# Optimization experiments

Measured on AMD Instinct MI355X. Metric: run time of the kernel, lower is better.

## Reference

```python
import jax, jax.numpy as jnp
import numpy as np

B, T, E, H, K, V = 256, 200, 100, 128, 13, 50000


def run_lstm(x, W, U, b, reverse=False):
    """Keras LSTM with activation=relu, recurrent_activation=sigmoid.
    x: [B,T,E]; W: [E,4H]; U: [H,4H]; b: [4H]. Gate order: i, f, g, o.
    Returns hidden states [B,T,H] (time-aligned for both directions)."""
    Bn = x.shape[0]
    Hn = U.shape[0]
    xw = jnp.einsum('bte,eg->btg', x, W) + b  # precompute input projections [B,T,4H]

    def step(carry, xw_t):
        h, c = carry
        z = xw_t + h @ U
        i, f, g, o = jnp.split(z, 4, axis=-1)
        i = jax.nn.sigmoid(i)
        f = jax.nn.sigmoid(f)
        g = jax.nn.relu(g)          # activation=relu (non-cuDNN path in TF)
        c = f * c + i * g
        h = o * jax.nn.relu(c)      # output activation also relu
        return (h, c), h

    init = (jnp.zeros((Bn, Hn), x.dtype), jnp.zeros((Bn, Hn), x.dtype))
    _, hs = jax.lax.scan(step, init, jnp.swapaxes(xw, 0, 1), reverse=reverse)
    return jnp.swapaxes(hs, 0, 1)


def crf_log_likelihood(logits, labels, lens, trans):
    """tfa.text.crf_log_likelihood: score(labels) - logZ, masked by seq lens."""
    Bn, Tn, Kn = logits.shape
    t_idx = jnp.arange(Tn)
    mask = t_idx[None, :] < lens[:, None]  # [B,T]
    # unary score
    unary = jnp.take_along_axis(logits, labels[..., None], axis=-1)[..., 0]
    u_score = jnp.sum(jnp.where(mask, unary, 0.0), axis=-1)
    # transition score
    pair = trans[labels[:, :-1], labels[:, 1:]]  # [B,T-1]
    pmask = t_idx[None, 1:] < lens[:, None]
    b_score = jnp.sum(jnp.where(pmask, pair, 0.0), axis=-1)
    # forward algorithm (log-space DP over time, masked updates)
    def step(alpha, inp):
        logit_t, valid = inp  # [B,K], [B]
        new = jax.nn.logsumexp(alpha[:, :, None] + trans[None], axis=1) + logit_t
        alpha = jnp.where(valid[:, None], new, alpha)
        return alpha, None

    alpha0 = logits[:, 0, :]
    xs = (jnp.swapaxes(logits[:, 1:, :], 0, 1), jnp.swapaxes(mask[:, 1:], 0, 1))
    alpha, _ = jax.lax.scan(step, alpha0, xs)
    logZ = jax.nn.logsumexp(alpha, axis=-1)
    return u_score + b_score - logZ


def setup_inputs() -> dict:
    key = jax.random.key(0)
    ks = jax.random.split(key, 12)
    s = lambda k, shape, sc: jax.random.normal(k, shape, jnp.float32) * sc
    return {
        'text': jax.random.randint(ks[0], (B, T), 0, V).astype(jnp.int32),
        'labels': jax.random.randint(ks[1], (B, T), 0, K).astype(jnp.int32),
        'emb': s(ks[2], (V, E), 0.1),
        'Wf': s(ks[3], (E, 4 * H), 0.05),
        'Uf': s(ks[4], (H, 4 * H), 0.05),
        'bf': jnp.zeros((4 * H,), jnp.float32),
        'Wb': s(ks[5], (E, 4 * H), 0.05),
        'Ub': s(ks[6], (H, 4 * H), 0.05),
        'bb': jnp.zeros((4 * H,), jnp.float32),
        'Wd': s(ks[7], (2 * H, K), 0.05),
        'bd': jnp.zeros((K,), jnp.float32),
        'trans': jax.random.uniform(ks[8], (K, K), jnp.float32),
    }


def reference(text, labels, emb, Wf, Uf, bf, Wb, Ub, bb, Wd, bd, trans):
    lens = jnp.sum((text != 0).astype(jnp.int32), axis=-1)  # [B]
    x = emb[text]                      # embedding lookup [B,T,E]
    # dropout is identity in eval mode
    h_fwd = run_lstm(x, Wf, Uf, bf, reverse=False)
    h_bwd = run_lstm(x, Wb, Ub, bb, reverse=True)
    h = jnp.concatenate([h_fwd, h_bwd], axis=-1)  # [B,T,2H]
    logits = jax.nn.softmax(h @ Wd + bd, axis=-1)  # Dense(softmax), per source
    log_likelihood = crf_log_likelihood(logits, labels, lens, trans)
    return logits, lens, log_likelihood
```

## Files before the change

kernel.cpp:

```cpp
#include <hip/hip_runtime.h>
#include <hip/hip_bf16.h>

#define Bn 256
#define Tn 200
#define En 100
#define Hn 128
#define Kn 13
#define G4 512
#define BT 51200

typedef __attribute__((ext_vector_type(8))) __bf16 bf8_t;
typedef __attribute__((ext_vector_type(4))) float f4_t;

__device__ __forceinline__ unsigned short f2bf(float f) {
  unsigned int u = __float_as_uint(f);
  u = (u + 0x7FFFu + ((u >> 16) & 1u)) >> 16;
  return (unsigned short)u;
}
__device__ __forceinline__ float bf2f(unsigned short s) {
  return __uint_as_float(((unsigned int)s) << 16);
}
__device__ __forceinline__ float sigm(float x) { return 1.f / (1.f + __expf(-x)); }

__device__ __forceinline__ void bar_lgkm() {
  asm volatile("s_waitcnt lgkmcnt(0)" ::: "memory");
  __builtin_amdgcn_s_barrier();
  __builtin_amdgcn_sched_barrier(0);
}

__device__ __forceinline__ int gperm(int n) {
  return ((n >> 4) & 3) * 128 + ((n >> 6) << 4) + (n & 15);
}

__global__ __launch_bounds__(256) void k_prep(const int* __restrict__ text,
                                              const float* __restrict__ Wf,
                                              const float* __restrict__ Wb,
                                              const float* __restrict__ Uf,
                                              const float* __restrict__ Ub,
                                              unsigned short* __restrict__ wt,
                                              unsigned short* __restrict__ ut,
                                              int* __restrict__ lens_i,
                                              float* __restrict__ out_lens) {
  int bx = blockIdx.x;
  if (bx < 1024) {
    int idx = bx * 256 + threadIdx.x;
    int half = idx >> 17;
    int rem = idx & 131071;
    int dir = rem >> 16;
    int nk = rem & 65535;
    int n = nk >> 7, k = nk & 127;
    int mc = gperm(n);
    if (half == 0) {
      const float* W = dir ? Wb : Wf;
      wt[rem] = f2bf((k < En) ? W[k * G4 + mc] : 0.f);
    } else {
      const float* U = dir ? Ub : Uf;
      ut[rem] = f2bf(U[k * G4 + mc]);
    }
  } else {
    int wi = threadIdx.x >> 6, lane = threadIdx.x & 63;
    int b = (bx - 1024) * 4 + wi;
    int cnt = 0;
    for (int t = lane; t < Tn; t += 64) cnt += (text[b * Tn + t] != 0);
    for (int off = 32; off; off >>= 1) cnt += __shfl_down(cnt, off);
    if (lane == 0) { lens_i[b] = cnt; out_lens[b] = (float)cnt; }
  }
}

#define FR16(M) M(0,0) M(0,1) M(0,2) M(0,3) M(1,0) M(1,1) M(1,2) M(1,3) \
                M(2,0) M(2,1) M(2,2) M(2,3) M(3,0) M(3,1) M(3,2) M(3,3)

__global__ __attribute__((amdgpu_flat_work_group_size(512, 512),
                          amdgpu_waves_per_eu(1, 2)))
void k_scan(const int* __restrict__ text,
            const float* __restrict__ emb,
            const unsigned short* __restrict__ wt,
            const unsigned short* __restrict__ ut,
            const float* __restrict__ biasf,
            const float* __restrict__ biasb,
            unsigned short* __restrict__ hf,
            unsigned short* __restrict__ hb) {
  int blk = blockIdx.x;
  int dir = blk >> 6;
  int bg = blk & 63;
  int b0 = bg * 4;
  int tid = threadIdx.x;
  int w = tid >> 6, l = tid & 63;
  int lr = l & 15, lg = l >> 4;
  int jj = w * 16 + lr;
  const unsigned short* ut_d = ut + (size_t)dir * (G4 * 128);
  const unsigned short* wt_d = wt + (size_t)dir * (G4 * 128);
  const float* bias = dir ? biasb : biasf;
  unsigned short* hout = dir ? hb : hf;
  int t0 = dir ? (Tn - 1) : 0;
  int dt = dir ? -1 : 1;

#define LOADUB(nt, kk) \
  bf8_t ub_##nt##_##kk = *(const bf8_t*)(ut_d + (size_t)(w * 64 + (nt) * 16 + lr) * 128 + (kk) * 32 + lg * 8); \
  asm volatile("" : "+a"(ub_##nt##_##kk));
  FR16(LOADUB)
#undef LOADUB
#define LOADWB(nt, kk) \
  bf8_t wb_##nt##_##kk = *(const bf8_t*)(wt_d + (size_t)(w * 64 + (nt) * 16 + lr) * 128 + (kk) * 32 + lg * 8); \
  asm volatile("" : "+a"(wb_##nt##_##kk));
  FR16(LOADWB)
#undef LOADWB

  __shared__ __align__(16) char lds_all[16384 + Tn * 4 * 4];
  char* lbase = lds_all;
  int* tl = (int*)(lds_all + 16384);
  for (int i = tid; i < 4096; i += 512) ((unsigned int*)lds_all)[i] = 0;
  #pragma unroll
  for (int r = 0; r < 4; r++)
    if (tid < Tn) tl[r * Tn + tid] = text[(size_t)(b0 + r) * Tn + tid];

  float bn0 = bias[gperm(w * 64 +  0 + lr)];
  float bn1 = bias[gperm(w * 64 + 16 + lr)];
  float bn2 = bias[gperm(w * 64 + 32 + lr)];
  float bn3 = bias[gperm(w * 64 + 48 + lr)];
  f4_t bv0 = {bn0, bn0, bn0, bn0};
  f4_t bv1 = {bn1, bn1, bn1, bn1};
  f4_t bv2 = {bn2, bn2, bn2, bn2};
  f4_t bv3 = {bn3, bn3, bn3, bn3};

  int xrow = tid >> 7;
  int xcol = tid & 127;
  bool xon = (xcol < En);
  float v0 = 0.f, v1 = 0.f, vA = 0.f, vB = 0.f;
  {
    const int* trow = text + (size_t)(b0 + xrow) * Tn;
    int k0 = trow[t0], k1 = trow[t0 + dt], k2 = trow[t0 + 2 * dt], k3 = trow[t0 + 3 * dt];
    if (xon) {
      v0 = emb[(size_t)k0 * En + xcol];
      v1 = emb[(size_t)k1 * En + xcol];
      vA = emb[(size_t)k2 * En + xcol];
      vB = emb[(size_t)k3 * En + xcol];
    }
  }

  int rb0 = (lr * 256 +   0 + lg * 16) ^ ((lr & 7) << 4);
  int rb1 = (lr * 256 +  64 + lg * 16) ^ ((lr & 7) << 4);
  int rb2 = (lr * 256 + 128 + lg * 16) ^ ((lr & 7) << 4);
  int rb3 = (lr * 256 + 192 + lg * 16) ^ ((lr & 7) << 4);
  int xb0 = 12288 + rb0, xb1 = 12288 + rb1, xb2 = 12288 + rb2, xb3 = 12288 + rb3;
  int wbh = (((lg * 4) * 256 + jj * 2) ^ (((lg * 4) & 7) << 4)) + 4096;
  int wbx = 8192 + (((xrow * 4) * 256 + xcol * 2) ^ (((xrow * 4) & 7) << 4));

  unsigned short* hp = hout + ((size_t)t0 * Bn + b0 + lg) * 128 + jj;
  const long long hstep = (long long)dt * Bn * 128;

  *(unsigned short*)(lbase + wbx) = f2bf(v0);
  *(unsigned short*)(lbase + (wbx ^ 4096)) = f2bf(v1);
  bar_lgkm();

  f4_t pA0 = bv0, pA1 = bv1, pA2 = bv2, pA3 = bv3;
  f4_t pB0, pB1, pB2, pB3;
  {
    bf8_t ax0 = *(const bf8_t*)(lbase + 8192 + rb0);
    bf8_t ax1 = *(const bf8_t*)(lbase + 8192 + rb1);
    bf8_t ax2 = *(const bf8_t*)(lbase + 8192 + rb2);
    bf8_t ax3 = *(const bf8_t*)(lbase + 8192 + rb3);
#define MFP(nt, kk) pA##nt = __builtin_amdgcn_mfma_f32_16x16x32_bf16(ax##kk, wb_##nt##_##kk, pA##nt, 0, 0, 0);
    MFP(0,0) MFP(1,0) MFP(2,0) MFP(3,0)
    MFP(0,1) MFP(1,1) MFP(2,1) MFP(3,1)
    MFP(0,2) MFP(1,2) MFP(2,2) MFP(3,2)
    MFP(0,3) MFP(1,3) MFP(2,3) MFP(3,3)
#undef MFP
  }
  float c0 = 0.f;
  int t = t0;

#define STEPF(P, Q) { \
    bf8_t af0 = *(const bf8_t*)(lbase + rb0); \
    bf8_t af1 = *(const bf8_t*)(lbase + rb1); \
    bf8_t af2 = *(const bf8_t*)(lbase + rb2); \
    bf8_t af3 = *(const bf8_t*)(lbase + rb3); \
     \
    *(unsigned short*)(lbase + wbx) = f2bf(vA); \
    vA = vB; \
    { int tc = t + 3 * dt; tc = tc < 0 ? 0 : (tc > Tn - 1 ? Tn - 1 : tc); \
      int tokN = tl[xrow * Tn + tc]; \
      vB = xon ? emb[(size_t)tokN * En + xcol] : 0.f; } \
     \
    P##0 = __builtin_amdgcn_mfma_f32_16x16x32_bf16(af0, ub_0_0, P##0, 0, 0, 0); \
    P##1 = __builtin_amdgcn_mfma_f32_16x16x32_bf16(af0, ub_1_0, P##1, 0, 0, 0); \
    P##2 = __builtin_amdgcn_mfma_f32_16x16x32_bf16(af0, ub_2_0, P##2, 0, 0, 0); \
    P##3 = __builtin_amdgcn_mfma_f32_16x16x32_bf16(af0, ub_3_0, P##3, 0, 0, 0); \
    P##0 = __builtin_amdgcn_mfma_f32_16x16x32_bf16(af1, ub_0_1, P##0, 0, 0, 0); \
    P##1 = __builtin_amdgcn_mfma_f32_16x16x32_bf16(af1, ub_1_1, P##1, 0, 0, 0); \
    P##2 = __builtin_amdgcn_mfma_f32_16x16x32_bf16(af1, ub_2_1, P##2, 0, 0, 0); \
    P##3 = __builtin_amdgcn_mfma_f32_16x16x32_bf16(af1, ub_3_1, P##3, 0, 0, 0); \
    P##0 = __builtin_amdgcn_mfma_f32_16x16x32_bf16(af2, ub_0_2, P##0, 0, 0, 0); \
    P##1 = __builtin_amdgcn_mfma_f32_16x16x32_bf16(af2, ub_1_2, P##1, 0, 0, 0); \
    P##2 = __builtin_amdgcn_mfma_f32_16x16x32_bf16(af2, ub_2_2, P##2, 0, 0, 0); \
    P##3 = __builtin_amdgcn_mfma_f32_16x16x32_bf16(af2, ub_3_2, P##3, 0, 0, 0); \
    P##0 = __builtin_amdgcn_mfma_f32_16x16x32_bf16(af3, ub_0_3, P##0, 0, 0, 0); \
    P##1 = __builtin_amdgcn_mfma_f32_16x16x32_bf16(af3, ub_1_3, P##1, 0, 0, 0); \
    P##2 = __builtin_amdgcn_mfma_f32_16x16x32_bf16(af3, ub_2_3, P##2, 0, 0, 0); \
    P##3 = __builtin_amdgcn_mfma_f32_16x16x32_bf16(af3, ub_3_3, P##3, 0, 0, 0); \
     \
    { bf8_t ax0 = *(const bf8_t*)(lbase + xb0); \
      bf8_t ax1 = *(const bf8_t*)(lbase + xb1); \
      bf8_t ax2 = *(const bf8_t*)(lbase + xb2); \
      bf8_t ax3 = *(const bf8_t*)(lbase + xb3); \
      Q##0 = bv0; Q##1 = bv1; Q##2 = bv2; Q##3 = bv3; \
      Q##0 = __builtin_amdgcn_mfma_f32_16x16x32_bf16(ax0, wb_0_0, Q##0, 0, 0, 0); \
      Q##1 = __builtin_amdgcn_mfma_f32_16x16x32_bf16(ax0, wb_1_0, Q##1, 0, 0, 0); \
      Q##2 = __builtin_amdgcn_mfma_f32_16x16x32_bf16(ax0, wb_2_0, Q##2, 0, 0, 0); \
      Q##3 = __builtin_amdgcn_mfma_f32_16x16x32_bf16(ax0, wb_3_0, Q##3, 0, 0, 0); \
      Q##0 = __builtin_amdgcn_mfma_f32_16x16x32_bf16(ax1, wb_0_1, Q##0, 0, 0, 0); \
      Q##1 = __builtin_amdgcn_mfma_f32_16x16x32_bf16(ax1, wb_1_1, Q##1, 0, 0, 0); \
      Q##2 = __builtin_amdgcn_mfma_f32_16x16x32_bf16(ax1, wb_2_1, Q##2, 0, 0, 0); \
      Q##3 = __builtin_amdgcn_mfma_f32_16x16x32_bf16(ax1, wb_3_1, Q##3, 0, 0, 0); \
      Q##0 = __builtin_amdgcn_mfma_f32_16x16x32_bf16(ax2, wb_0_2, Q##0, 0, 0, 0); \
      Q##1 = __builtin_amdgcn_mfma_f32_16x16x32_bf16(ax2, wb_1_2, Q##1, 0, 0, 0); \
      Q##2 = __builtin_amdgcn_mfma_f32_16x16x32_bf16(ax2, wb_2_2, Q##2, 0, 0, 0); \
      Q##3 = __builtin_amdgcn_mfma_f32_16x16x32_bf16(ax2, wb_3_2, Q##3, 0, 0, 0); \
      Q##0 = __builtin_amdgcn_mfma_f32_16x16x32_bf16(ax3, wb_0_3, Q##0, 0, 0, 0); \
      Q##1 = __builtin_amdgcn_mfma_f32_16x16x32_bf16(ax3, wb_1_3, Q##1, 0, 0, 0); \
      Q##2 = __builtin_amdgcn_mfma_f32_16x16x32_bf16(ax3, wb_2_3, Q##2, 0, 0, 0); \
      Q##3 = __builtin_amdgcn_mfma_f32_16x16x32_bf16(ax3, wb_3_3, Q##3, 0, 0, 0); } \
     \
    float ig = sigm(P##0[0]); \
    float fg = sigm(P##1[0]); \
    float gg = fmaxf(P##2[0], 0.f); \
    c0 = fmaf(fg, c0, ig * gg); \
    unsigned short hs2 = f2bf(sigm(P##3[0]) * fmaxf(c0, 0.f)); \
    *(unsigned short*)(lbase + wbh) = hs2; \
    bar_lgkm(); \
    hp[0] = hs2; \
    rb0 ^= 4096; rb1 ^= 4096; rb2 ^= 4096; rb3 ^= 4096; \
    xb0 ^= 4096; xb1 ^= 4096; xb2 ^= 4096; xb3 ^= 4096; \
    wbh ^= 4096; wbx ^= 4096; \
    hp += hstep; \
    t += dt; }

  for (int tt = 0; tt < Tn; tt += 2) {
    STEPF(pA, pB)
    STEPF(pB, pA)
  }
#undef STEPF
}

__global__ __launch_bounds__(128) void k_logits(const unsigned short* __restrict__ hf,
                                                const unsigned short* __restrict__ hb,
                                                const float* __restrict__ Wd,
                                                const float* __restrict__ bd,
                                                float* __restrict__ out) {
  __shared__ unsigned short hs[128 * 256];
  int tid = threadIdx.x;
  size_t row0 = (size_t)blockIdx.x * 128;
  #pragma unroll
  for (int it = 0; it < 16; it++) {
    int idx = it * 128 + tid;
    int r = idx >> 4, c = idx & 15;
    bf8_t vf = *(const bf8_t*)(hf + (row0 + r) * 128 + c * 8);
    bf8_t vb = *(const bf8_t*)(hb + (row0 + r) * 128 + c * 8);
    int byte = (r * 512 + c * 16) ^ ((r & 7) << 4);
    *(bf8_t*)((char*)hs + byte) = vf;
    int byte2 = (r * 512 + 256 + c * 16) ^ ((r & 7) << 4);
    *(bf8_t*)((char*)hs + byte2) = vb;
  }
  __syncthreads();
  float acc[Kn];
  #pragma unroll
  for (int jj = 0; jj < Kn; jj++) acc[jj] = bd[jj];
  int r = tid;
  #pragma unroll 4
  for (int c = 0; c < 32; c++) {
    int byte = (r * 512 + c * 16) ^ ((r & 7) << 4);
    bf8_t v = *(const bf8_t*)((const char*)hs + byte);
    #pragma unroll
    for (int e = 0; e < 8; e++) {
      float h = (float)v[e];
      int k = c * 8 + e;
      #pragma unroll
      for (int jj = 0; jj < Kn; jj++)
        acc[jj] = fmaf(h, Wd[k * Kn + jj], acc[jj]);
    }
  }
  float m = acc[0];
  #pragma unroll
  for (int jj = 1; jj < Kn; jj++) m = fmaxf(m, acc[jj]);
  float s = 0.f;
  #pragma unroll
  for (int jj = 0; jj < Kn; jj++) { acc[jj] = __expf(acc[jj] - m); s += acc[jj]; }
  float inv = 1.f / s;
  int rg = (int)row0 + tid;
  int b = rg & 255, t = rg >> 8;
  float* op = out + ((size_t)b * Tn + t) * Kn;
  #pragma unroll
  for (int jj = 0; jj < Kn; jj++) op[jj] = acc[jj] * inv;
}

__global__ __launch_bounds__(64) void k_crf(const float* __restrict__ logits,
                                            const int* __restrict__ labels,
                                            const int* __restrict__ lens_i,
                                            const float* __restrict__ trans,
                                            float* __restrict__ out_ll) {
  int b = blockIdx.x, lane = threadIdx.x;
  int len = lens_i[b];
  const float* lg = logits + (size_t)b * Tn * Kn;
  const int* lab = labels + (size_t)b * Tn;
  float sc = 0.f;
  for (int t = lane; t < Tn; t += 64) {
    if (t < len) {
      sc += lg[t * Kn + lab[t]];
      if (t >= 1) sc += trans[lab[t - 1] * Kn + lab[t]];
    }
  }
  for (int off = 32; off; off >>= 1) sc += __shfl_down(sc, off);
  bool act = lane < Kn;
  int jl = act ? lane : 0;
  float etr[Kn];
  #pragma unroll
  for (int i = 0; i < Kn; i++) etr[i] = __expf(trans[i * Kn + jl]);
  float a = act ? lg[jl] : -INFINITY;
  float lgv = (len > 1) ? lg[Kn + jl] : 0.f;
  for (int t = 1; t < len; t++) {
    float lgn = (t + 1 < len) ? lg[(t + 1) * Kn + jl] : 0.f;
    float m = a;
    for (int off = 8; off; off >>= 1) m = fmaxf(m, __shfl_xor(m, off, 16));
    float ea = __expf(a - m);
    float s = 0.f;
    #pragma unroll
    for (int i = 0; i < Kn; i++) s = fmaf(__shfl(ea, i), etr[i], s);
    float anew = m + __logf(s) + lgv;
    if (act) a = anew;
    lgv = lgn;
  }
  float m2 = a;
  for (int off = 8; off; off >>= 1) m2 = fmaxf(m2, __shfl_xor(m2, off, 16));
  float ea2 = act ? __expf(a - m2) : 0.f;
  float ssum = ea2;
  for (int off = 8; off; off >>= 1) ssum += __shfl_xor(ssum, off, 16);
  float logZ = m2 + __logf(ssum);
  if (lane == 0) out_ll[b] = sc - logZ;
}

extern "C" void kernel_launch(void* const* d_in, const int* in_sizes, int n_in,
                              void* d_out, int out_size, void* d_ws, size_t ws_size,
                              hipStream_t stream) {
  const int* text = (const int*)d_in[0];
  const int* labels = (const int*)d_in[1];
  const float* emb = (const float*)d_in[2];
  const float* Wf = (const float*)d_in[3];
  const float* Uf = (const float*)d_in[4];
  const float* bf_ = (const float*)d_in[5];
  const float* Wb = (const float*)d_in[6];
  const float* Ub = (const float*)d_in[7];
  const float* bb_ = (const float*)d_in[8];
  const float* Wd = (const float*)d_in[9];
  const float* bd = (const float*)d_in[10];
  const float* trans = (const float*)d_in[11];
  (void)in_sizes; (void)n_in; (void)out_size; (void)ws_size;

  float* out = (float*)d_out;
  float* out_logits = out;
  float* out_lens = out + (size_t)BT * Kn;
  float* out_ll = out_lens + Bn;

  char* ws = (char*)d_ws;
  size_t o = 0;
  int* lens_i = (int*)(ws + o);                o += 1024;
  unsigned short* wt = (unsigned short*)(ws + o);  o += (size_t)2 * G4 * 128 * 2;
  unsigned short* ut = (unsigned short*)(ws + o);  o += (size_t)2 * G4 * 128 * 2;
  unsigned short* hfb = (unsigned short*)(ws + o); o += (size_t)BT * Hn * 2;
  unsigned short* hbb = (unsigned short*)(ws + o); o += (size_t)BT * Hn * 2;

  hipLaunchKernelGGL(k_prep, dim3(1088), dim3(256), 0, stream,
                     text, Wf, Wb, Uf, Ub, wt, ut, lens_i, out_lens);
  hipLaunchKernelGGL(k_scan, dim3(128), dim3(512), 0, stream,
                     text, emb, wt, ut, bf_, bb_, hfb, hbb);
  hipLaunchKernelGGL(k_logits, dim3(400), dim3(128), 0, stream, hfb, hbb, Wd, bd, out_logits);
  hipLaunchKernelGGL(k_crf, dim3(Bn), dim3(64), 0, stream, out_logits, labels, lens_i, trans, out_ll);
}
```

Before: 285.2 us.

## Halve scan block to 4 waves, each computing 8 gate tiles

The LSTM scan kernel now runs with 256 threads per block instead of 512. Each wave covers 32 hidden units, using 8 MFMA N-tiles with doubled U and W register fragments, and each thread handles two embedding rows. The aim is to cut the per-step barrier cost across fewer waves and give each wave more independent MFMA chains to hide latency. In exchange, each wave carries twice the serial MFMA and activation work per step and much higher register pressure (64 bf8 weight fragments).

Measured after the change: 326.8 us. +14.6%, slower.

```diff
diff --git a/kernel.cpp b/kernel.cpp
--- a/kernel.cpp
+++ b/kernel.cpp
@@ -31,6 +31,8 @@
 __device__ __forceinline__ int gperm(int n) {
   return ((n >> 4) & 3) * 128 + ((n >> 6) << 4) + (n & 15);
 }
+
+#define MFMA(a, b, c) __builtin_amdgcn_mfma_f32_16x16x32_bf16(a, b, c, 0, 0, 0)
 
 __global__ __launch_bounds__(256) void k_prep(const int* __restrict__ text,
                                               const float* __restrict__ Wf,
@@ -67,11 +69,43 @@
   }
 }
 
-#define FR16(M) M(0,0) M(0,1) M(0,2) M(0,3) M(1,0) M(1,1) M(1,2) M(1,3) \
-                M(2,0) M(2,1) M(2,2) M(2,3) M(3,0) M(3,1) M(3,2) M(3,3)
-
-__global__ __attribute__((amdgpu_flat_work_group_size(512, 512),
-                          amdgpu_waves_per_eu(1, 2)))
+#define NT8K4(M) M(0,0) M(0,1) M(0,2) M(0,3) M(1,0) M(1,1) M(1,2) M(1,3) \
+                 M(2,0) M(2,1) M(2,2) M(2,3) M(3,0) M(3,1) M(3,2) M(3,3) \
+                 M(4,0) M(4,1) M(4,2) M(4,3) M(5,0) M(5,1) M(5,2) M(5,3) \
+                 M(6,0) M(6,1) M(6,2) M(6,3) M(7,0) M(7,1) M(7,2) M(7,3)
+
+#define MFUK(P, kk) \
+    P##0 = MFMA(af##kk, ub_0_##kk, P##0); \
+    P##1 = MFMA(af##kk, ub_1_##kk, P##1); \
+    P##2 = MFMA(af##kk, ub_2_##kk, P##2); \
+    P##3 = MFMA(af##kk, ub_3_##kk, P##3); \
+    P##4 = MFMA(af##kk, ub_4_##kk, P##4); \
+    P##5 = MFMA(af##kk, ub_5_##kk, P##5); \
+    P##6 = MFMA(af##kk, ub_6_##kk, P##6); \
+    P##7 = MFMA(af##kk, ub_7_##kk, P##7);
+
+#define MFW0(Q) \
+    Q##0 = MFMA(ax0, wb_0_0, bv0); \
+    Q##1 = MFMA(ax0, wb_1_0, bv1); \
+    Q##2 = MFMA(ax0, wb_2_0, bv2); \
+    Q##3 = MFMA(ax0, wb_3_0, bv3); \
+    Q##4 = MFMA(ax0, wb_4_0, bv4); \
+    Q##5 = MFMA(ax0, wb_5_0, bv5); \
+    Q##6 = MFMA(ax0, wb_6_0, bv6); \
+    Q##7 = MFMA(ax0, wb_7_0, bv7);
+
+#define MFWK(Q, kk) \
+    Q##0 = MFMA(ax##kk, wb_0_##kk, Q##0); \
+    Q##1 = MFMA(ax##kk, wb_1_##kk, Q##1); \
+    Q##2 = MFMA(ax##kk, wb_2_##kk, Q##2); \
+    Q##3 = MFMA(ax##kk, wb_3_##kk, Q##3); \
+    Q##4 = MFMA(ax##kk, wb_4_##kk, Q##4); \
+    Q##5 = MFMA(ax##kk, wb_5_##kk, Q##5); \
+    Q##6 = MFMA(ax##kk, wb_6_##kk, Q##6); \
+    Q##7 = MFMA(ax##kk, wb_7_##kk, Q##7);
+
+__global__ __attribute__((amdgpu_flat_work_group_size(256, 256),
+                          amdgpu_waves_per_eu(1, 1)))
 void k_scan(const int* __restrict__ text,
             const float* __restrict__ emb,
             const unsigned short* __restrict__ wt,
@@ -87,7 +121,7 @@
   int tid = threadIdx.x;
   int w = tid >> 6, l = tid & 63;
   int lr = l & 15, lg = l >> 4;
-  int jj = w * 16 + lr;
+  int j0 = w * 32 + lr;
   const unsigned short* ut_d = ut + (size_t)dir * (G4 * 128);
   const unsigned short* wt_d = wt + (size_t)dir * (G4 * 128);
   const float* bias = dir ? biasb : biasf;
@@ -96,45 +130,49 @@
   int dt = dir ? -1 : 1;
 
 #define LOADUB(nt, kk) \
-  bf8_t ub_##nt##_##kk = *(const bf8_t*)(ut_d + (size_t)(w * 64 + (nt) * 16 + lr) * 128 + (kk) * 32 + lg * 8); \
+  bf8_t ub_##nt##_##kk = *(const bf8_t*)(ut_d + (size_t)(w * 128 + (nt) * 16 + lr) * 128 + (kk) * 32 + lg * 8); \
   asm volatile("" : "+a"(ub_##nt##_##kk));
-  FR16(LOADUB)
+  NT8K4(LOADUB)
 #undef LOADUB
 #define LOADWB(nt, kk) \
-  bf8_t wb_##nt##_##kk = *(const bf8_t*)(wt_d + (size_t)(w * 64 + (nt) * 16 + lr) * 128 + (kk) * 32 + lg * 8); \
+  bf8_t wb_##nt##_##kk = *(const bf8_t*)(wt_d + (size_t)(w * 128 + (nt) * 16 + lr) * 128 + (kk) * 32 + lg * 8); \
   asm volatile("" : "+a"(wb_##nt##_##kk));
-  FR16(LOADWB)
+  NT8K4(LOADWB)
 #undef LOADWB
 
   __shared__ __align__(16) char lds_all[16384 + Tn * 4 * 4];
   char* lbase = lds_all;
   int* tl = (int*)(lds_all + 16384);
-  for (int i = tid; i < 4096; i += 512) ((unsigned int*)lds_all)[i] = 0;
+  for (int i = tid; i < 4096; i += 256) ((unsigned int*)lds_all)[i] = 0;
   #pragma unroll
   for (int r = 0; r < 4; r++)
     if (tid < Tn) tl[r * Tn + tid] = text[(size_t)(b0 + r) * Tn + tid];
 
-  float bn0 = bias[gperm(w * 64 +  0 + lr)];
-  float bn1 = bias[gperm(w * 64 + 16 + lr)];
-  float bn2 = bias[gperm(w * 64 + 32 + lr)];
-  float bn3 = bias[gperm(w * 64 + 48 + lr)];
-  f4_t bv0 = {bn0, bn0, bn0, bn0};
-  f4_t bv1 = {bn1, bn1, bn1, bn1};
-  f4_t bv2 = {bn2, bn2, bn2, bn2};
-  f4_t bv3 = {bn3, bn3, bn3, bn3};
-
-  int xrow = tid >> 7;
-  int xcol = tid & 127;
-  bool xon = (xcol < En);
-  float v0 = 0.f, v1 = 0.f, vA = 0.f, vB = 0.f;
+  f4_t bv0, bv1, bv2, bv3, bv4, bv5, bv6, bv7;
+#define LBIAS(nt) { float b_ = bias[gperm(w * 128 + (nt) * 16 + lr)]; \
+  bv##nt[0] = b_; bv##nt[1] = b_; bv##nt[2] = b_; bv##nt[3] = b_; }
+  LBIAS(0) LBIAS(1) LBIAS(2) LBIAS(3) LBIAS(4) LBIAS(5) LBIAS(6) LBIAS(7)
+#undef LBIAS
+
+  int xr0 = tid >> 7;
+  int xc = tid & 127;
+  bool xon = (xc < En);
+  float v00 = 0.f, v01 = 0.f;
+  float v10 = 0.f, v11 = 0.f;
+  float vA0 = 0.f, vA1 = 0.f;
+  float vB0 = 0.f, vB1 = 0.f;
   {
-    const int* trow = text + (size_t)(b0 + xrow) * Tn;
-    int k0 = trow[t0], k1 = trow[t0 + dt], k2 = trow[t0 + 2 * dt], k3 = trow[t0 + 3 * dt];
+    const int* tr0 = text + (size_t)(b0 + xr0) * Tn;
+    const int* tr1 = text + (size_t)(b0 + xr0 + 2) * Tn;
     if (xon) {
-      v0 = emb[(size_t)k0 * En + xcol];
-      v1 = emb[(size_t)k1 * En + xcol];
-      vA = emb[(size_t)k2 * En + xcol];
-      vB = emb[(size_t)k3 * En + xcol];
+      v00 = emb[(size_t)tr0[t0] * En + xc];
+      v01 = emb[(size_t)tr1[t0] * En + xc];
+      v10 = emb[(size_t)tr0[t0 + dt] * En + xc];
+      v11 = emb[(size_t)tr1[t0 + dt] * En + xc];
+      vA0 = emb[(size_t)tr0[t0 + 2 * dt] * En + xc];
+      vA1 = emb[(size_t)tr1[t0 + 2 * dt] * En + xc];
+      vB0 = emb[(size_t)tr0[t0 + 3 * dt] * En + xc];
+      vB1 = emb[(size_t)tr1[t0 + 3 * dt] * En + xc];
     }
   }
 
@@ -143,31 +181,34 @@
   int rb2 = (lr * 256 + 128 + lg * 16) ^ ((lr & 7) << 4);
   int rb3 = (lr * 256 + 192 + lg * 16) ^ ((lr & 7) << 4);
   int xb0 = 12288 + rb0, xb1 = 12288 + rb1, xb2 = 12288 + rb2, xb3 = 12288 + rb3;
-  int wbh = (((lg * 4) * 256 + jj * 2) ^ (((lg * 4) & 7) << 4)) + 4096;
-  int wbx = 8192 + (((xrow * 4) * 256 + xcol * 2) ^ (((xrow * 4) & 7) << 4));
-
-  unsigned short* hp = hout + ((size_t)t0 * Bn + b0 + lg) * 128 + jj;
+  int hrow = lg * 4;
+  int hsw = ((hrow & 7) << 4);
+  int wbh0 = ((hrow * 256 + j0 * 2) ^ hsw) + 4096;
+  int wbh1 = ((hrow * 256 + (j0 + 16) * 2) ^ hsw) + 4096;
+  int xrow0b = (xr0 * 4) * 256;
+  int xrow1b = ((xr0 + 2) * 4) * 256;
+  int wbx0 = 8192 + ((xrow0b + xc * 2) ^ (((xr0 * 4) & 7) << 4));
+  int wbx1 = 8192 + ((xrow1b + xc * 2) ^ ((((xr0 + 2) * 4) & 7) << 4));
+
+  unsigned short* hp = hout + ((size_t)t0 * Bn + b0 + lg) * 128 + j0;
   const long long hstep = (long long)dt * Bn * 128;
 
-  *(unsigned short*)(lbase + wbx) = f2bf(v0);
-  *(unsigned short*)(lbase + (wbx ^ 4096)) = f2bf(v1);
+  *(unsigned short*)(lbase + wbx0) = f2bf(v00);
+  *(unsigned short*)(lbase + wbx1) = f2bf(v01);
+  *(unsigned short*)(lbase + (wbx0 ^ 4096)) = f2bf(v10);
+  *(unsigned short*)(lbase + (wbx1 ^ 4096)) = f2bf(v11);
   bar_lgkm();
 
-  f4_t pA0 = bv0, pA1 = bv1, pA2 = bv2, pA3 = bv3;
-  f4_t pB0, pB1, pB2, pB3;
+  f4_t pA0, pA1, pA2, pA3, pA4, pA5, pA6, pA7;
+  f4_t pB0, pB1, pB2, pB3, pB4, pB5, pB6, pB7;
   {
     bf8_t ax0 = *(const bf8_t*)(lbase + 8192 + rb0);
     bf8_t ax1 = *(const bf8_t*)(lbase + 8192 + rb1);
     bf8_t ax2 = *(const bf8_t*)(lbase + 8192 + rb2);
     bf8_t ax3 = *(const bf8_t*)(lbase + 8192 + rb3);
-#define MFP(nt, kk) pA##nt = __builtin_amdgcn_mfma_f32_16x16x32_bf16(ax##kk, wb_##nt##_##kk, pA##nt, 0, 0, 0);
-    MFP(0,0) MFP(1,0) MFP(2,0) MFP(3,0)
-    MFP(0,1) MFP(1,1) MFP(2,1) MFP(3,1)
-    MFP(0,2) MFP(1,2) MFP(2,2) MFP(3,2)
-    MFP(0,3) MFP(1,3) MFP(2,3) MFP(3,3)
-#undef MFP
-  }
-  float c0 = 0.f;
+    MFW0(pA) MFWK(pA, 1) MFWK(pA, 2) MFWK(pA, 3)
+  }
+  float c0 = 0.f, c1 = 0.f;
   int t = t0;
 
 #define STEPF(P, Q) { \
@@ -175,63 +216,41 @@
     bf8_t af1 = *(const bf8_t*)(lbase + rb1); \
     bf8_t af2 = *(const bf8_t*)(lbase + rb2); \
     bf8_t af3 = *(const bf8_t*)(lbase + rb3); \
+    bf8_t ax0 = *(const bf8_t*)(lbase + xb0); \
+    bf8_t ax1 = *(const bf8_t*)(lbase + xb1); \
+    bf8_t ax2 = *(const bf8_t*)(lbase + xb2); \
+    bf8_t ax3 = *(const bf8_t*)(lbase + xb3); \
      \
-    *(unsigned short*)(lbase + wbx) = f2bf(vA); \
-    vA = vB; \
+    *(unsigned short*)(lbase + wbx0) = f2bf(vA0); \
+    *(unsigned short*)(lbase + wbx1) = f2bf(vA1); \
+    vA0 = vB0; vA1 = vB1; \
     { int tc = t + 3 * dt; tc = tc < 0 ? 0 : (tc > Tn - 1 ? Tn - 1 : tc); \
-      int tokN = tl[xrow * Tn + tc]; \
-      vB = xon ? emb[(size_t)tokN * En + xcol] : 0.f; } \
+      int tk0 = tl[xr0 * Tn + tc]; \
+      int tk1 = tl[(xr0 + 2) * Tn + tc]; \
+      vB0 = xon ? emb[(size_t)tk0 * En + xc] : 0.f; \
+      vB1 = xon ? emb[(size_t)tk1 * En + xc] : 0.f; } \
      \
-    P##0 = __builtin_amdgcn_mfma_f32_16x16x32_bf16(af0, ub_0_0, P##0, 0, 0, 0); \
-    P##1 = __builtin_amdgcn_mfma_f32_16x16x32_bf16(af0, ub_1_0, P##1, 0, 0, 0); \
-    P##2 = __builtin_amdgcn_mfma_f32_16x16x32_bf16(af0, ub_2_0, P##2, 0, 0, 0); \
-    P##3 = __builtin_amdgcn_mfma_f32_16x16x32_bf16(af0, ub_3_0, P##3, 0, 0, 0); \
-    P##0 = __builtin_amdgcn_mfma_f32_16x16x32_bf16(af1, ub_0_1, P##0, 0, 0, 0); \
-    P##1 = __builtin_amdgcn_mfma_f32_16x16x32_bf16(af1, ub_1_1, P##1, 0, 0, 0); \
-    P##2 = __builtin_amdgcn_mfma_f32_16x16x32_bf16(af1, ub_2_1, P##2, 0, 0, 0); \
-    P##3 = __builtin_amdgcn_mfma_f32_16x16x32_bf16(af1, ub_3_1, P##3, 0, 0, 0); \
-    P##0 = __builtin_amdgcn_mfma_f32_16x16x32_bf16(af2, ub_0_2, P##0, 0, 0, 0); \
-    P##1 = __builtin_amdgcn_mfma_f32_16x16x32_bf16(af2, ub_1_2, P##1, 0, 0, 0); \
-    P##2 = __builtin_amdgcn_mfma_f32_16x16x32_bf16(af2, ub_2_2, P##2, 0, 0, 0); \
-    P##3 = __builtin_amdgcn_mfma_f32_16x16x32_bf16(af2, ub_3_2, P##3, 0, 0, 0); \
-    P##0 = __builtin_amdgcn_mfma_f32_16x16x32_bf16(af3, ub_0_3, P##0, 0, 0, 0); \
-    P##1 = __builtin_amdgcn_mfma_f32_16x16x32_bf16(af3, ub_1_3, P##1, 0, 0, 0); \
-    P##2 = __builtin_amdgcn_mfma_f32_16x16x32_bf16(af3, ub_2_3, P##2, 0, 0, 0); \
-    P##3 = __builtin_amdgcn_mfma_f32_16x16x32_bf16(af3, ub_3_3, P##3, 0, 0, 0); \
+    MFUK(P, 0) MFUK(P, 1) MFUK(P, 2) MFUK(P, 3) \
      \
-    { bf8_t ax0 = *(const bf8_t*)(lbase + xb0); \
-      bf8_t ax1 = *(const bf8_t*)(lbase + xb1); \
-      bf8_t ax2 = *(const bf8_t*)(lbase + xb2); \
-      bf8_t ax3 = *(const bf8_t*)(lbase + xb3); \
-      Q##0 = bv0; Q##1 = bv1; Q##2 = bv2; Q##3 = bv3; \
-      Q##0 = __builtin_amdgcn_mfma_f32_16x16x32_bf16(ax0, wb_0_0, Q##0, 0, 0, 0); \
-      Q##1 = __builtin_amdgcn_mfma_f32_16x16x32_bf16(ax0, wb_1_0, Q##1, 0, 0, 0); \
-      Q##2 = __builtin_amdgcn_mfma_f32_16x16x32_bf16(ax0, wb_2_0, Q##2, 0, 0, 0); \
-      Q##3 = __builtin_amdgcn_mfma_f32_16x16x32_bf16(ax0, wb_3_0, Q##3, 0, 0, 0); \
-      Q##0 = __builtin_amdgcn_mfma_f32_16x16x32_bf16(ax1, wb_0_1, Q##0, 0, 0, 0); \
-      Q##1 = __builtin_amdgcn_mfma_f32_16x16x32_bf16(ax1, wb_1_1, Q##1, 0, 0, 0); \
-      Q##2 = __builtin_amdgcn_mfma_f32_16x16x32_bf16(ax1, wb_2_1, Q##2, 0, 0, 0); \
-      Q##3 = __builtin_amdgcn_mfma_f32_16x16x32_bf16(ax1, wb_3_1, Q##3, 0, 0, 0); \
-      Q##0 = __builtin_amdgcn_mfma_f32_16x16x32_bf16(ax2, wb_0_2, Q##0, 0, 0, 0); \
-      Q##1 = __builtin_amdgcn_mfma_f32_16x16x32_bf16(ax2, wb_1_2, Q##1, 0, 0, 0); \
-      Q##2 = __builtin_amdgcn_mfma_f32_16x16x32_bf16(ax2, wb_2_2, Q##2, 0, 0, 0); \
-      Q##3 = __builtin_amdgcn_mfma_f32_16x16x32_bf16(ax2, wb_3_2, Q##3, 0, 0, 0); \
-      Q##0 = __builtin_amdgcn_mfma_f32_16x16x32_bf16(ax3, wb_0_3, Q##0, 0, 0, 0); \
-      Q##1 = __builtin_amdgcn_mfma_f32_16x16x32_bf16(ax3, wb_1_3, Q##1, 0, 0, 0); \
-      Q##2 = __builtin_amdgcn_mfma_f32_16x16x32_bf16(ax3, wb_2_3, Q##2, 0, 0, 0); \
-      Q##3 = __builtin_amdgcn_mfma_f32_16x16x32_bf16(ax3, wb_3_3, Q##3, 0, 0, 0); } \
+    MFW0(Q) MFWK(Q, 1) MFWK(Q, 2) MFWK(Q, 3) \
      \
-    float ig = sigm(P##0[0]); \
-    float fg = sigm(P##1[0]); \
-    float gg = fmaxf(P##2[0], 0.f); \
-    c0 = fmaf(fg, c0, ig * gg); \
-    unsigned short hs2 = f2bf(sigm(P##3[0]) * fmaxf(c0, 0.f)); \
-    *(unsigned short*)(lbase + wbh) = hs2; \
+    float ig0 = sigm(P##0[0]); \
+    float fg0 = sigm(P##1[0]); \
+    float gg0 = fmaxf(P##2[0], 0.f); \
+    c0 = fmaf(fg0, c0, ig0 * gg0); \
+    unsigned short h0s = f2bf(sigm(P##3[0]) * fmaxf(c0, 0.f)); \
+    float ig1 = sigm(P##4[0]); \
+    float fg1 = sigm(P##5[0]); \
+    float gg1 = fmaxf(P##6[0], 0.f); \
+    c1 = fmaf(fg1, c1, ig1 * gg1); \
+    unsigned short h1s = f2bf(sigm(P##7[0]) * fmaxf(c1, 0.f)); \
+    *(unsigned short*)(lbase + wbh0) = h0s; \
+    *(unsigned short*)(lbase + wbh1) = h1s; \
     bar_lgkm(); \
-    hp[0] = hs2; \
+    hp[0] = h0s; hp[16] = h1s; \
     rb0 ^= 4096; rb1 ^= 4096; rb2 ^= 4096; rb3 ^= 4096; \
     xb0 ^= 4096; xb1 ^= 4096; xb2 ^= 4096; xb3 ^= 4096; \
-    wbh ^= 4096; wbx ^= 4096; \
+    wbh0 ^= 4096; wbh1 ^= 4096; wbx0 ^= 4096; wbx1 ^= 4096; \
     hp += hstep; \
     t += dt; }
 
@@ -370,7 +389,7 @@
 
   hipLaunchKernelGGL(k_prep, dim3(1088), dim3(256), 0, stream,
                      text, Wf, Wb, Uf, Ub, wt, ut, lens_i, out_lens);
-  hipLaunchKernelGGL(k_scan, dim3(128), dim3(512), 0, stream,
+  hipLaunchKernelGGL(k_scan, dim3(128), dim3(256), 0, stream,
                      text, emb, wt, ut, bf_, bb_, hfb, hbb);
   hipLaunchKernelGGL(k_logits, dim3(400), dim3(128), 0, stream, hfb, hbb, Wd, bd, out_logits);
   hipLaunchKernelGGL(k_crf, dim3(Bn), dim3(64), 0, stream, out_logits, labels, lens_i, trans, out_ll);
```

## Pregather bf16 embeddings in prep kernel and load x fragments directly in scan

Applied to the files above, without the earlier changes.

The prep kernel now gathers embedding rows for every (t,b) into a padded bf16 buffer laid out time-major. The scan kernel reads its MFMA A-fragments for the input projection straight from global memory, prefetched two steps ahead in registers. This drops the per-step embedding gather, the LDS staging writes and reads of x, and the token table from the serial recurrence loop. In exchange it adds an extra 13 MB write and read pass plus a larger prep launch, and it raises register pressure in the scan kernel.

New measurement: 303.0 us. 6.2% more time.

```diff
diff --git a/kernel.cpp b/kernel.cpp
--- a/kernel.cpp
+++ b/kernel.cpp
@@ -32,13 +32,17 @@
   return ((n >> 4) & 3) * 128 + ((n >> 6) << 4) + (n & 15);
 }
 
+#define MFMA(a, b, c) __builtin_amdgcn_mfma_f32_16x16x32_bf16(a, b, c, 0, 0, 0)
+
 __global__ __launch_bounds__(256) void k_prep(const int* __restrict__ text,
+                                              const float* __restrict__ emb,
                                               const float* __restrict__ Wf,
                                               const float* __restrict__ Wb,
                                               const float* __restrict__ Uf,
                                               const float* __restrict__ Ub,
                                               unsigned short* __restrict__ wt,
                                               unsigned short* __restrict__ ut,
+                                              unsigned short* __restrict__ xg,
                                               int* __restrict__ lens_i,
                                               float* __restrict__ out_lens) {
   int bx = blockIdx.x;
@@ -57,13 +61,28 @@
       const float* U = dir ? Ub : Uf;
       ut[rem] = f2bf(U[k * G4 + mc]);
     }
-  } else {
+  } else if (bx < 1088) {
     int wi = threadIdx.x >> 6, lane = threadIdx.x & 63;
     int b = (bx - 1024) * 4 + wi;
     int cnt = 0;
     for (int t = lane; t < Tn; t += 64) cnt += (text[b * Tn + t] != 0);
     for (int off = 32; off; off >>= 1) cnt += __shfl_down(cnt, off);
     if (lane == 0) { lens_i[b] = cnt; out_lens[b] = (float)cnt; }
+  } else {
+    int row = (bx - 1088) * 128 + (threadIdx.x >> 1);
+    int half = threadIdx.x & 1;
+    int b = row & 255, t = row >> 8;
+    int tok = text[(size_t)b * Tn + t];
+    const float* er = emb + (size_t)tok * En;
+    unsigned short* xr = xg + (size_t)row * 128 + half * 64;
+    #pragma unroll
+    for (int c = 0; c < 64; c += 2) {
+      int col = half * 64 + c;
+      float v0 = (col < En) ? er[col] : 0.f;
+      float v1 = (col + 1 < En) ? er[col + 1] : 0.f;
+      unsigned int pk = (unsigned int)f2bf(v0) | ((unsigned int)f2bf(v1) << 16);
+      *(unsigned int*)(xr + c) = pk;
+    }
   }
 }
 
@@ -72,8 +91,7 @@
 
 __global__ __attribute__((amdgpu_flat_work_group_size(512, 512),
                           amdgpu_waves_per_eu(1, 2)))
-void k_scan(const int* __restrict__ text,
-            const float* __restrict__ emb,
+void k_scan(const unsigned short* __restrict__ xg,
             const unsigned short* __restrict__ wt,
             const unsigned short* __restrict__ ut,
             const float* __restrict__ biasf,
@@ -106,13 +124,9 @@
   FR16(LOADWB)
 #undef LOADWB
 
-  __shared__ __align__(16) char lds_all[16384 + Tn * 4 * 4];
+  __shared__ __align__(16) char lds_all[8192];
   char* lbase = lds_all;
-  int* tl = (int*)(lds_all + 16384);
-  for (int i = tid; i < 4096; i += 512) ((unsigned int*)lds_all)[i] = 0;
-  #pragma unroll
-  for (int r = 0; r < 4; r++)
-    if (tid < Tn) tl[r * Tn + tid] = text[(size_t)(b0 + r) * Tn + tid];
+  for (int i = tid; i < 2048; i += 512) ((unsigned int*)lds_all)[i] = 0;
 
   float bn0 = bias[gperm(w * 64 +  0 + lr)];
   float bn1 = bias[gperm(w * 64 + 16 + lr)];
@@ -123,103 +137,94 @@
   f4_t bv2 = {bn2, bn2, bn2, bn2};
   f4_t bv3 = {bn3, bn3, bn3, bn3};
 
-  int xrow = tid >> 7;
-  int xcol = tid & 127;
-  bool xon = (xcol < En);
-  float v0 = 0.f, v1 = 0.f, vA = 0.f, vB = 0.f;
-  {
-    const int* trow = text + (size_t)(b0 + xrow) * Tn;
-    int k0 = trow[t0], k1 = trow[t0 + dt], k2 = trow[t0 + 2 * dt], k3 = trow[t0 + 3 * dt];
-    if (xon) {
-      v0 = emb[(size_t)k0 * En + xcol];
-      v1 = emb[(size_t)k1 * En + xcol];
-      vA = emb[(size_t)k2 * En + xcol];
-      vB = emb[(size_t)k3 * En + xcol];
-    }
-  }
+  const unsigned short* xrow = xg + ((size_t)(b0 + (lr >> 2))) * 128 + lg * 8;
+  const size_t xtstep = (size_t)Bn * 128;
+
+#define XLOAD(XF, TQ) { int tc = (TQ); tc = tc < 0 ? 0 : (tc > Tn - 1 ? Tn - 1 : tc); \
+    const unsigned short* xp = xrow + (size_t)tc * xtstep; \
+    XF##0 = *(const bf8_t*)(xp); \
+    XF##1 = *(const bf8_t*)(xp + 32); \
+    XF##2 = *(const bf8_t*)(xp + 64); \
+    XF##3 = *(const bf8_t*)(xp + 96); }
 
   int rb0 = (lr * 256 +   0 + lg * 16) ^ ((lr & 7) << 4);
   int rb1 = (lr * 256 +  64 + lg * 16) ^ ((lr & 7) << 4);
   int rb2 = (lr * 256 + 128 + lg * 16) ^ ((lr & 7) << 4);
   int rb3 = (lr * 256 + 192 + lg * 16) ^ ((lr & 7) << 4);
-  int xb0 = 12288 + rb0, xb1 = 12288 + rb1, xb2 = 12288 + rb2, xb3 = 12288 + rb3;
   int wbh = (((lg * 4) * 256 + jj * 2) ^ (((lg * 4) & 7) << 4)) + 4096;
-  int wbx = 8192 + (((xrow * 4) * 256 + xcol * 2) ^ (((xrow * 4) & 7) << 4));
 
   unsigned short* hp = hout + ((size_t)t0 * Bn + b0 + lg) * 128 + jj;
   const long long hstep = (long long)dt * Bn * 128;
 
-  *(unsigned short*)(lbase + wbx) = f2bf(v0);
-  *(unsigned short*)(lbase + (wbx ^ 4096)) = f2bf(v1);
-  bar_lgkm();
-
-  f4_t pA0 = bv0, pA1 = bv1, pA2 = bv2, pA3 = bv3;
+  f4_t pA0, pA1, pA2, pA3;
   f4_t pB0, pB1, pB2, pB3;
-  {
-    bf8_t ax0 = *(const bf8_t*)(lbase + 8192 + rb0);
-    bf8_t ax1 = *(const bf8_t*)(lbase + 8192 + rb1);
-    bf8_t ax2 = *(const bf8_t*)(lbase + 8192 + rb2);
-    bf8_t ax3 = *(const bf8_t*)(lbase + 8192 + rb3);
-#define MFP(nt, kk) pA##nt = __builtin_amdgcn_mfma_f32_16x16x32_bf16(ax##kk, wb_##nt##_##kk, pA##nt, 0, 0, 0);
-    MFP(0,0) MFP(1,0) MFP(2,0) MFP(3,0)
-    MFP(0,1) MFP(1,1) MFP(2,1) MFP(3,1)
-    MFP(0,2) MFP(1,2) MFP(2,2) MFP(3,2)
-    MFP(0,3) MFP(1,3) MFP(2,3) MFP(3,3)
-#undef MFP
-  }
+  bf8_t xp0, xp1, xp2, xp3;
+  XLOAD(xp, t0)
+  pA0 = MFMA(xp0, wb_0_0, bv0);
+  pA1 = MFMA(xp0, wb_1_0, bv1);
+  pA2 = MFMA(xp0, wb_2_0, bv2);
+  pA3 = MFMA(xp0, wb_3_0, bv3);
+  pA0 = MFMA(xp1, wb_0_1, pA0);
+  pA1 = MFMA(xp1, wb_1_1, pA1);
+  pA2 = MFMA(xp1, wb_2_1, pA2);
+  pA3 = MFMA(xp1, wb_3_1, pA3);
+  pA0 = MFMA(xp2, wb_0_2, pA0);
+  pA1 = MFMA(xp2, wb_1_2, pA1);
+  pA2 = MFMA(xp2, wb_2_2, pA2);
+  pA3 = MFMA(xp2, wb_3_2, pA3);
+  pA0 = MFMA(xp3, wb_0_3, pA0);
+  pA1 = MFMA(xp3, wb_1_3, pA1);
+  pA2 = MFMA(xp3, wb_2_3, pA2);
+  pA3 = MFMA(xp3, wb_3_3, pA3);
+  bf8_t xfA0, xfA1, xfA2, xfA3;
+  bf8_t xfB0, xfB1, xfB2, xfB3;
+  XLOAD(xfA, t0 + dt)
+  XLOAD(xfB, t0 + 2 * dt)
   float c0 = 0.f;
   int t = t0;
-
-#define STEPF(P, Q) { \
+  bar_lgkm();
+
+#define STEPF(P, Q, XF) { \
     bf8_t af0 = *(const bf8_t*)(lbase + rb0); \
     bf8_t af1 = *(const bf8_t*)(lbase + rb1); \
     bf8_t af2 = *(const bf8_t*)(lbase + rb2); \
     bf8_t af3 = *(const bf8_t*)(lbase + rb3); \
      \
-    *(unsigned short*)(lbase + wbx) = f2bf(vA); \
-    vA = vB; \
-    { int tc = t + 3 * dt; tc = tc < 0 ? 0 : (tc > Tn - 1 ? Tn - 1 : tc); \
-      int tokN = tl[xrow * Tn + tc]; \
-      vB = xon ? emb[(size_t)tokN * En + xcol] : 0.f; } \
+    P##0 = MFMA(af0, ub_0_0, P##0); \
+    P##1 = MFMA(af0, ub_1_0, P##1); \
+    P##2 = MFMA(af0, ub_2_0, P##2); \
+    P##3 = MFMA(af0, ub_3_0, P##3); \
+    P##0 = MFMA(af1, ub_0_1, P##0); \
+    P##1 = MFMA(af1, ub_1_1, P##1); \
+    P##2 = MFMA(af1, ub_2_1, P##2); \
+    P##3 = MFMA(af1, ub_3_1, P##3); \
+    P##0 = MFMA(af2, ub_0_2, P##0); \
+    P##1 = MFMA(af2, ub_1_2, P##1); \
+    P##2 = MFMA(af2, ub_2_2, P##2); \
+    P##3 = MFMA(af2, ub_3_2, P##3); \
+    P##0 = MFMA(af3, ub_0_3, P##0); \
+    P##1 = MFMA(af3, ub_1_3, P##1); \
+    P##2 = MFMA(af3, ub_2_3, P##2); \
+    P##3 = MFMA(af3, ub_3_3, P##3); \
      \
-    P##0 = __builtin_amdgcn_mfma_f32_16x16x32_bf16(af0, ub_0_0, P##0, 0, 0, 0); \
-    P##1 = __builtin_amdgcn_mfma_f32_16x16x32_bf16(af0, ub_1_0, P##1, 0, 0, 0); \
-    P##2 = __builtin_amdgcn_mfma_f32_16x16x32_bf16(af0, ub_2_0, P##2, 0, 0, 0); \
-    P##3 = __builtin_amdgcn_mfma_f32_16x16x32_bf16(af0, ub_3_0, P##3, 0, 0, 0); \
-    P##0 = __builtin_amdgcn_mfma_f32_16x16x32_bf16(af1, ub_0_1, P##0, 0, 0, 0); \
-    P##1 = __builtin_amdgcn_mfma_f32_16x16x32_bf16(af1, ub_1_1, P##1, 0, 0, 0); \
-    P##2 = __builtin_amdgcn_mfma_f32_16x16x32_bf16(af1, ub_2_1, P##2, 0, 0, 0); \
-    P##3 = __builtin_amdgcn_mfma_f32_16x16x32_bf16(af1, ub_3_1, P##3, 0, 0, 0); \
-    P##0 = __builtin_amdgcn_mfma_f32_16x16x32_bf16(af2, ub_0_2, P##0, 0, 0, 0); \
-    P##1 = __builtin_amdgcn_mfma_f32_16x16x32_bf16(af2, ub_1_2, P##1, 0, 0, 0); \
-    P##2 = __builtin_amdgcn_mfma_f32_16x16x32_bf16(af2, ub_2_2, P##2, 0, 0, 0); \
-    P##3 = __builtin_amdgcn_mfma_f32_16x16x32_bf16(af2, ub_3_2, P##3, 0, 0, 0); \
-    P##0 = __builtin_amdgcn_mfma_f32_16x16x32_bf16(af3, ub_0_3, P##0, 0, 0, 0); \
-    P##1 = __builtin_amdgcn_mfma_f32_16x16x32_bf16(af3, ub_1_3, P##1, 0, 0, 0); \
-    P##2 = __builtin_amdgcn_mfma_f32_16x16x32_bf16(af3, ub_2_3, P##2, 0, 0, 0); \
-    P##3 = __builtin_amdgcn_mfma_f32_16x16x32_bf16(af3, ub_3_3, P##3, 0, 0, 0); \
+    Q##0 = MFMA(XF##0, wb_0_0, bv0); \
+    Q##1 = MFMA(XF##0, wb_1_0, bv1); \
+    Q##2 = MFMA(XF##0, wb_2_0, bv2); \
+    Q##3 = MFMA(XF##0, wb_3_0, bv3); \
+    Q##0 = MFMA(XF##1, wb_0_1, Q##0); \
+    Q##1 = MFMA(XF##1, wb_1_1, Q##1); \
+    Q##2 = MFMA(XF##1, wb_2_1, Q##2); \
+    Q##3 = MFMA(XF##1, wb_3_1, Q##3); \
+    Q##0 = MFMA(XF##2, wb_0_2, Q##0); \
+    Q##1 = MFMA(XF##2, wb_1_2, Q##1); \
+    Q##2 = MFMA(XF##2, wb_2_2, Q##2); \
+    Q##3 = MFMA(XF##2, wb_3_2, Q##3); \
+    Q##0 = MFMA(XF##3, wb_0_3, Q##0); \
+    Q##1 = MFMA(XF##3, wb_1_3, Q##1); \
+    Q##2 = MFMA(XF##3, wb_2_3, Q##2); \
+    Q##3 = MFMA(XF##3, wb_3_3, Q##3); \
      \
-    { bf8_t ax0 = *(const bf8_t*)(lbase + xb0); \
-      bf8_t ax1 = *(const bf8_t*)(lbase + xb1); \
-      bf8_t ax2 = *(const bf8_t*)(lbase + xb2); \
-      bf8_t ax3 = *(const bf8_t*)(lbase + xb3); \
-      Q##0 = bv0; Q##1 = bv1; Q##2 = bv2; Q##3 = bv3; \
-      Q##0 = __builtin_amdgcn_mfma_f32_16x16x32_bf16(ax0, wb_0_0, Q##0, 0, 0, 0); \
-      Q##1 = __builtin_amdgcn_mfma_f32_16x16x32_bf16(ax0, wb_1_0, Q##1, 0, 0, 0); \
-      Q##2 = __builtin_amdgcn_mfma_f32_16x16x32_bf16(ax0, wb_2_0, Q##2, 0, 0, 0); \
-      Q##3 = __builtin_amdgcn_mfma_f32_16x16x32_bf16(ax0, wb_3_0, Q##3, 0, 0, 0); \
-      Q##0 = __builtin_amdgcn_mfma_f32_16x16x32_bf16(ax1, wb_0_1, Q##0, 0, 0, 0); \
-      Q##1 = __builtin_amdgcn_mfma_f32_16x16x32_bf16(ax1, wb_1_1, Q##1, 0, 0, 0); \
-      Q##2 = __builtin_amdgcn_mfma_f32_16x16x32_bf16(ax1, wb_2_1, Q##2, 0, 0, 0); \
-      Q##3 = __builtin_amdgcn_mfma_f32_16x16x32_bf16(ax1, wb_3_1, Q##3, 0, 0, 0); \
-      Q##0 = __builtin_amdgcn_mfma_f32_16x16x32_bf16(ax2, wb_0_2, Q##0, 0, 0, 0); \
-      Q##1 = __builtin_amdgcn_mfma_f32_16x16x32_bf16(ax2, wb_1_2, Q##1, 0, 0, 0); \
-      Q##2 = __builtin_amdgcn_mfma_f32_16x16x32_bf16(ax2, wb_2_2, Q##2, 0, 0, 0); \
-      Q##3 = __builtin_amdgcn_mfma_f32_16x16x32_bf16(ax2, wb_3_2, Q##3, 0, 0, 0); \
-      Q##0 = __builtin_amdgcn_mfma_f32_16x16x32_bf16(ax3, wb_0_3, Q##0, 0, 0, 0); \
-      Q##1 = __builtin_amdgcn_mfma_f32_16x16x32_bf16(ax3, wb_1_3, Q##1, 0, 0, 0); \
-      Q##2 = __builtin_amdgcn_mfma_f32_16x16x32_bf16(ax3, wb_2_3, Q##2, 0, 0, 0); \
-      Q##3 = __builtin_amdgcn_mfma_f32_16x16x32_bf16(ax3, wb_3_3, Q##3, 0, 0, 0); } \
+    XLOAD(XF, t + 3 * dt) \
      \
     float ig = sigm(P##0[0]); \
     float fg = sigm(P##1[0]); \
@@ -230,16 +235,16 @@
     bar_lgkm(); \
     hp[0] = hs2; \
     rb0 ^= 4096; rb1 ^= 4096; rb2 ^= 4096; rb3 ^= 4096; \
-    xb0 ^= 4096; xb1 ^= 4096; xb2 ^= 4096; xb3 ^= 4096; \
-    wbh ^= 4096; wbx ^= 4096; \
+    wbh ^= 4096; \
     hp += hstep; \
     t += dt; }
 
   for (int tt = 0; tt < Tn; tt += 2) {
-    STEPF(pA, pB)
-    STEPF(pB, pA)
+    STEPF(pA, pB, xfA)
+    STEPF(pB, pA, xfB)
   }
 #undef STEPF
+#undef XLOAD
 }
 
 __global__ __launch_bounds__(128) void k_logits(const unsigned short* __restrict__ hf,
@@ -365,13 +370,14 @@
   int* lens_i = (int*)(ws + o);                o += 1024;
   unsigned short* wt = (unsigned short*)(ws + o);  o += (size_t)2 * G4 * 128 * 2;
   unsigned short* ut = (unsigned short*)(ws + o);  o += (size_t)2 * G4 * 128 * 2;
+  unsigned short* xg = (unsigned short*)(ws + o);  o += (size_t)BT * 128 * 2;
   unsigned short* hfb = (unsigned short*)(ws + o); o += (size_t)BT * Hn * 2;
   unsigned short* hbb = (unsigned short*)(ws + o); o += (size_t)BT * Hn * 2;
 
-  hipLaunchKernelGGL(k_prep, dim3(1088), dim3(256), 0, stream,
-                     text, Wf, Wb, Uf, Ub, wt, ut, lens_i, out_lens);
+  hipLaunchKernelGGL(k_prep, dim3(1488), dim3(256), 0, stream,
+                     text, emb, Wf, Wb, Uf, Ub, wt, ut, xg, lens_i, out_lens);
   hipLaunchKernelGGL(k_scan, dim3(128), dim3(512), 0, stream,
-                     text, emb, wt, ut, bf_, bb_, hfb, hbb);
+                     xg, wt, ut, bf_, bb_, hfb, hbb);
   hipLaunchKernelGGL(k_logits, dim3(400), dim3(128), 0, stream, hfb, hbb, Wd, bd, out_logits);
   hipLaunchKernelGGL(k_crf, dim3(Bn), dim3(64), 0, stream, out_logits, labels, lens_i, trans, out_ll);
 }
```
